# Performance work log

Hardware: AMD Instinct MI355X
Metric: run time of the kernel (lower is better)

Reference implementation:

```python
import jax, jax.numpy as jnp
import numpy as np

N_MODES = 64


def setup_inputs() -> dict:
    key = jax.random.key(0)
    k1, k2, k3 = jax.random.split(key, 3)
    B, Cin, S = 32, 128, 8192
    H, Hc, M = 4, 32, N_MODES  # n_heads, head_channels, n_modes (Cout = H*Hc = 128)
    x = jax.random.normal(k1, (B, Cin, S), dtype=jnp.float32)
    # per-head init scale: std = 0.01 * 2**h (matches _init_weights)
    scale = (0.01 * 2.0 ** jnp.arange(H, dtype=jnp.float32)).reshape(H, 1, 1, 1)
    w_real = jax.random.normal(k2, (H, Cin, Hc, M), dtype=jnp.float32) * scale
    w_imag = jax.random.normal(k3, (H, Cin, Hc, M), dtype=jnp.float32) * scale
    return {"x": x, "w_real": w_real, "w_imag": w_imag}


def reference(x, w_real, w_imag):
    B, Cin, S = x.shape
    H, _, Hc, M = w_real.shape
    Cout = H * Hc
    x_ft = jnp.fft.rfft(x, axis=-1)                 # [B, Cin, F] complex64
    F = x_ft.shape[-1]
    M = min(M, F)                                    # static
    w = (w_real + 1j * w_imag).astype(x_ft.dtype)    # [H, Cin, Hc, M]
    # fused batched complex contraction over all heads/modes at once
    out = jnp.einsum('bim,hiom->bhom', x_ft[:, :, :M], w[..., :M])  # [B, H, Hc, M]
    out = out.reshape(B, Cout, M)                    # head h -> channels [h*Hc, (h+1)*Hc)
    out_ft = jnp.zeros((B, Cout, F), dtype=x_ft.dtype).at[:, :, :M].set(out)
    return jnp.fft.irfft(out_ft, n=S, axis=-1)       # [B, Cout, S] float32
```

## Files before the change

### kernel.cpp

```cpp
#include <hip/hip_runtime.h>
#include <cstdio>

#define S_LEN 8192
#define NM 64

typedef short s8v __attribute__((ext_vector_type(8)));
typedef float f4  __attribute__((ext_vector_type(4)));
typedef _Float16 h8 __attribute__((ext_vector_type(8)));

static __device__ inline unsigned short f2bf(float f) {
    unsigned int u = __builtin_bit_cast(unsigned int, f);
    u = (u + 0x7FFFu + ((u >> 16) & 1u)) >> 16;
    return (unsigned short)u;
}
static __device__ inline float bf2f(unsigned short h) {
    unsigned int u = ((unsigned int)h) << 16;
    return __builtin_bit_cast(float, u);
}

#define SW32(r, k) (((r) * 32) + ((k) ^ ((((r) >> 1) & 3) << 3)))

static __device__ __forceinline__ void glds16(const void* g, void* l) {
    __builtin_amdgcn_global_load_lds(
        (const __attribute__((address_space(1))) unsigned int*)g,
        (__attribute__((address_space(3))) unsigned int*)l, 16, 0, 0);
}

__global__ __launch_bounds__(256) void gen_master(float* __restrict__ tab) {
    int p = blockIdx.x * 256 + threadIdx.x;
    tab[p] = cosf((float)p * (6.28318530717958647692f / (float)S_LEN));
}

__global__ __launch_bounds__(256) void gen_t1_img(const float* __restrict__ tab,
                                                  short* __restrict__ Th,
                                                  short* __restrict__ Tl) {
    int tid = blockIdx.x * 256 + threadIdx.x;
    int tile = tid >> 12;
    int sb = tile >> 2, kc = tile & 3;
    int us = tid & 4095;
    int ls = us >> 5, kx = us & 31;
    int lk = kx ^ (((ls >> 1) & 3) << 3);
    int s = sb * 128 + ls;
    int k = kc * 32 + lk;
    int m = k >> 1;
    int p = (m * s + ((k & 1) << 11)) & (S_LEN - 1);
    float v = tab[p];
    unsigned short h = f2bf(v);
    Th[tid] = (short)h;
    Tl[tid] = (short)f2bf(v - bf2f(h));
}

__global__ __launch_bounds__(256) void gen_b_img(const float* __restrict__ tab,
                                                 _Float16* __restrict__ Bimg) {
    int tid = blockIdx.x * 256 + threadIdx.x;
    int tk = tid >> 13;
    int us = tid & 8191;
    int c = us >> 6;
    int wl = us & 63;
    int slot = wl >> 3, e = wl & 7;
    int k = ((slot ^ (c & 7)) << 3) | e;
    int kg = tk * 64 + k;
    int m = c >> 1;
    int p = (m * kg + ((c & 1) << 11)) & (S_LEN - 1);
    Bimg[tid] = (_Float16)tab[p];
}

__global__ __launch_bounds__(512, 4) void dft_fwd_mfma(const float* __restrict__ x,
        const _Float16* __restrict__ Bimg, float* __restrict__ P) {
    __shared__ _Float16 abh[2][4096], abl[2][4096];
    __shared__ _Float16 bb[2][8192];
    const int t = threadIdx.x;
    const int lane = t & 63, w = t >> 6;
    const int rl = lane & 15, kq = lane >> 4;
    const int wr = w >> 2, wc = w & 3;
    const int row0 = blockIdx.x * 64;
    const int ks = blockIdx.y;
    const int rA = t >> 3, sA = t & 7;
    const size_t xrow = (size_t)(row0 + rA) * S_LEN + (size_t)ks * 1024 + (size_t)sA * 8;
    const int usA = rA * 64 + ((sA ^ (rA & 7)) << 3);
    const size_t bby = (size_t)ks * 16 * 16384 + (size_t)t * 32;

    f4 acc[2][2];
    #pragma unroll
    for (int i = 0; i < 2; ++i)
        #pragma unroll
        for (int j = 0; j < 2; ++j) acc[i][j] = (f4){0.f, 0.f, 0.f, 0.f};

    f4 aP[3][2];
    h8 bP[2][2];

    #define LA_(SC, A0, A1) { A0 = *(const f4*)&x[xrow + (size_t)(SC) * 64];       \
                              A1 = *(const f4*)&x[xrow + (size_t)(SC) * 64 + 4]; }
    #define LB_(SC, B0, B1) { const char* g = (const char*)Bimg + bby +            \
                                  (size_t)(SC) * 16384;                            \
                              B0 = *(const h8*)g; B1 = *(const h8*)(g + 16); }
    #define CV_(A0, A1, NXT) { h8 hv, lv;                                          \
        _Pragma("unroll")                                                          \
        for (int e = 0; e < 4; ++e) {                                              \
            float f = A0[e]; _Float16 hh = (_Float16)f;                            \
            hv[e] = hh; lv[e] = (_Float16)(f - (float)hh);                         \
        }                                                                          \
        _Pragma("unroll")                                                          \
        for (int e = 0; e < 4; ++e) {                                              \
            float f = A1[e]; _Float16 hh = (_Float16)f;                            \
            hv[4 + e] = hh; lv[4 + e] = (_Float16)(f - (float)hh);                 \
        }                                                                          \
        *(h8*)&abh[NXT][usA] = hv;                                                 \
        *(h8*)&abl[NXT][usA] = lv; }
    #define WB_(B0, B1, NXT) { *(h8*)&bb[NXT][t * 16] = B0;                        \
                               *(h8*)&bb[NXT][t * 16 + 8] = B1; }
    #define MM_(CUR) { _Pragma("unroll")                                           \
        for (int ksl = 0; ksl < 2; ++ksl) {                                        \
            const int sb_ = ksl * 4 + kq;                                          \
            h8 Ah0, Al0, Ah1, Al1, Bv0, Bv1;                                       \
            { int r = wr * 32 + rl;      int u = r * 64 + ((sb_ ^ (r & 7)) << 3);  \
              Ah0 = *(const h8*)&abh[CUR][u]; Al0 = *(const h8*)&abl[CUR][u]; }    \
            { int r = wr * 32 + 16 + rl; int u = r * 64 + ((sb_ ^ (r & 7)) << 3);  \
              Ah1 = *(const h8*)&abh[CUR][u]; Al1 = *(const h8*)&abl[CUR][u]; }    \
            { int c = wc * 32 + rl;      int u = c * 64 + ((sb_ ^ (c & 7)) << 3);  \
              Bv0 = *(const h8*)&bb[CUR][u]; }                                     \
            { int c = wc * 32 + 16 + rl; int u = c * 64 + ((sb_ ^ (c & 7)) << 3);  \
              Bv1 = *(const h8*)&bb[CUR][u]; }                                     \
            acc[0][0] = __builtin_amdgcn_mfma_f32_16x16x32_f16(Ah0, Bv0, acc[0][0], 0, 0, 0); \
            acc[0][1] = __builtin_amdgcn_mfma_f32_16x16x32_f16(Ah0, Bv1, acc[0][1], 0, 0, 0); \
            acc[1][0] = __builtin_amdgcn_mfma_f32_16x16x32_f16(Ah1, Bv0, acc[1][0], 0, 0, 0); \
            acc[1][1] = __builtin_amdgcn_mfma_f32_16x16x32_f16(Ah1, Bv1, acc[1][1], 0, 0, 0); \
            acc[0][0] = __builtin_amdgcn_mfma_f32_16x16x32_f16(Al0, Bv0, acc[0][0], 0, 0, 0); \
            acc[0][1] = __builtin_amdgcn_mfma_f32_16x16x32_f16(Al0, Bv1, acc[0][1], 0, 0, 0); \
            acc[1][0] = __builtin_amdgcn_mfma_f32_16x16x32_f16(Al1, Bv0, acc[1][0], 0, 0, 0); \
            acc[1][1] = __builtin_amdgcn_mfma_f32_16x16x32_f16(Al1, Bv1, acc[1][1], 0, 0, 0); \
        } }
    #define BAR_ __builtin_amdgcn_sched_barrier(0);                                \
        asm volatile("s_waitcnt lgkmcnt(0)" ::: "memory");                         \
        __builtin_amdgcn_sched_barrier(0);                                         \
        __builtin_amdgcn_s_barrier();                                              \
        __builtin_amdgcn_sched_barrier(0);

    {
        f4 t0a, t0b; h8 tb0a, tb0b;
        LA_(0, t0a, t0b) LB_(0, tb0a, tb0b)
        LA_(1, aP[1][0], aP[1][1]) LA_(2, aP[2][0], aP[2][1])
        LB_(1, bP[1][0], bP[1][1])
        __builtin_amdgcn_sched_barrier(0);
        CV_(t0a, t0b, 0) WB_(tb0a, tb0b, 0)
        BAR_
    }
    #pragma unroll
    for (int s = 0; s < 16; ++s) {
        if (s + 3 <= 15) LA_(s + 3, aP[(s + 3) % 3][0], aP[(s + 3) % 3][1])
        if (s + 2 <= 15) LB_(s + 2, bP[(s + 2) & 1][0], bP[(s + 2) & 1][1])
        __builtin_amdgcn_sched_barrier(0);
        if (s + 1 <= 15) { CV_(aP[(s + 1) % 3][0], aP[(s + 1) % 3][1], (s + 1) & 1)
                           WB_(bP[(s + 1) & 1][0], bP[(s + 1) & 1][1], (s + 1) & 1) }
        MM_(s & 1)
        if (s < 15) { BAR_ }
    }

    float* Pks = P + (size_t)ks * 524288;
    #pragma unroll
    for (int mf = 0; mf < 2; ++mf)
        #pragma unroll
        for (int nf = 0; nf < 2; ++nf)
            #pragma unroll
            for (int r = 0; r < 4; ++r)
                Pks[(size_t)(row0 + wr * 32 + mf * 16 + kq * 4 + r) * 128
                    + wc * 32 + nf * 16 + rl] = acc[mf][nf][r];
}

__global__ __launch_bounds__(256) void ksum(const float* __restrict__ P,
                                            float* __restrict__ X) {
    int i = (blockIdx.x * 256 + threadIdx.x) * 4;
    f4 s = (f4){0.f, 0.f, 0.f, 0.f};
    #pragma unroll
    for (int ks = 0; ks < 8; ++ks)
        s += *(const f4*)&P[(size_t)ks * 524288 + i];
    *(f4*)&X[i] = s;
}

__global__ __launch_bounds__(256) void mode_contract(const float* __restrict__ X,
        const float* __restrict__ w_real, const float* __restrict__ w_imag,
        short* __restrict__ C2h, short* __restrict__ C2l) {
    __shared__ float xr[32][128], xi[32][128];
    __shared__ float wr[128][32], wi[128][32];
    const int m = blockIdx.x, h = blockIdx.y, t = threadIdx.x;
    #pragma unroll
    for (int it = 0; it < 16; ++it) {
        int li = t + it * 256;
        int b = li >> 7, i = li & 127;
        const float2 v = *(const float2*)&X[(size_t)(b * 128 + i) * 128 + 2 * m];
        xr[b][i] = v.x; xi[b][i] = v.y;
        int i2 = li >> 5, o = li & 31;
        size_t off = ((size_t)((h * 128 + i2) * 32 + o)) * NM + m;
        wr[i2][o] = w_real[off];
        wi[i2][o] = w_imag[off];
    }
    __syncthreads();
    const int o = t & 31;
    const int b0 = (t >> 5) * 4;
    float re[4] = {0.f, 0.f, 0.f, 0.f}, im[4] = {0.f, 0.f, 0.f, 0.f};
    for (int i = 0; i < 128; ++i) {
        float wrv = wr[i][o], wiv = wi[i][o];
        #pragma unroll
        for (int j = 0; j < 4; ++j) {
            float a = xr[b0 + j][i], c = xi[b0 + j][i];
            re[j] += a * wrv - c * wiv;
            im[j] += a * wiv + c * wrv;
        }
    }
    const float alpha = (m == 0) ? (1.0f / (float)S_LEN) : (2.0f / (float)S_LEN);
    const int kc = m >> 4;
    const int lk = (2 * m) & 31;
    #pragma unroll
    for (int j = 0; j < 4; ++j) {
        int row = (b0 + j) * 128 + h * 32 + o;
        float vr = alpha * re[j], vi = alpha * im[j];
        unsigned short hr = f2bf(vr), hi_ = f2bf(vi);
        float lr = vr - bf2f(hr), li_ = vi - bf2f(hi_);
        int rb = row >> 7, lr_ = row & 127;
        size_t ui = ((size_t)(rb * 4 + kc) * 4096 + SW32(lr_, lk)) >> 1;
        ((unsigned int*)C2h)[ui] = ((unsigned int)hi_ << 16) | hr;
        ((unsigned int*)C2l)[ui] = ((unsigned int)f2bf(li_) << 16) | f2bf(lr);
    }
}

__global__ __launch_bounds__(256, 2) void idft_mfma(const short* __restrict__ C2h,
        const short* __restrict__ C2l, const short* __restrict__ T1h,
        const short* __restrict__ T1l, float* __restrict__ y) {
    __shared__ short ah[2][4096], al[2][4096];
    __shared__ short bh[2][4096], bl[2][4096];
    const int t = threadIdx.x;
    const int lane = t & 63, wid = t >> 6;
    const int wm = (wid >> 1) * 64, wn = (wid & 1) * 64;
    const int sb = blockIdx.x;
    const int rb = blockIdx.y;
    f4 acc[4][4];
    #pragma unroll
    for (int i = 0; i < 4; ++i)
        #pragma unroll
        for (int j = 0; j < 4; ++j) acc[i][j] = (f4){0.f, 0.f, 0.f, 0.f};

    #define DMA3(kc, buf)  {                                                       \
        const size_t ta = (size_t)(rb * 4 + (kc)) * 8192;                          \
        const size_t tb = (size_t)(sb * 4 + (kc)) * 8192;                          \
        const int wo = wid * 2048 + lane * 16;                                     \
        glds16((const char*)C2h + ta + wo,        (char*)&ah[buf][0] + wid * 2048);        \
        glds16((const char*)C2h + ta + wo + 1024, (char*)&ah[buf][0] + wid * 2048 + 1024); \
        glds16((const char*)C2l + ta + wo,        (char*)&al[buf][0] + wid * 2048);        \
        glds16((const char*)C2l + ta + wo + 1024, (char*)&al[buf][0] + wid * 2048 + 1024); \
        glds16((const char*)T1h + tb + wo,        (char*)&bh[buf][0] + wid * 2048);        \
        glds16((const char*)T1h + tb + wo + 1024, (char*)&bh[buf][0] + wid * 2048 + 1024); \
        glds16((const char*)T1l + tb + wo,        (char*)&bl[buf][0] + wid * 2048);        \
        glds16((const char*)T1l + tb + wo + 1024, (char*)&bl[buf][0] + wid * 2048 + 1024); }

    DMA3(0, 0);
    __syncthreads();
    #pragma unroll
    for (int kc = 0; kc < 4; ++kc) {
        const int cur = kc & 1;
        if (kc < 3) DMA3(kc + 1, cur ^ 1);
        {
            const int kk = (lane >> 4) * 8, rl = lane & 15;
            s8v Ah[4], Al[4], Bh[4], Bl[4];
            #pragma unroll
            for (int mf = 0; mf < 4; ++mf) {
                int us = SW32(wm + mf * 16 + rl, kk);
                Ah[mf] = *(const s8v*)&ah[cur][us];
                Al[mf] = *(const s8v*)&al[cur][us];
            }
            #pragma unroll
            for (int nf = 0; nf < 4; ++nf) {
                int us = SW32(wn + nf * 16 + rl, kk);
                Bh[nf] = *(const s8v*)&bh[cur][us];
                Bl[nf] = *(const s8v*)&bl[cur][us];
            }
            #pragma unroll
            for (int mf = 0; mf < 4; ++mf)
                #pragma unroll
                for (int nf = 0; nf < 4; ++nf)
                    acc[mf][nf] = __builtin_amdgcn_mfma_f32_16x16x32_bf16(Ah[mf], Bh[nf], acc[mf][nf], 0, 0, 0);
            #pragma unroll
            for (int mf = 0; mf < 4; ++mf)
                #pragma unroll
                for (int nf = 0; nf < 4; ++nf)
                    acc[mf][nf] = __builtin_amdgcn_mfma_f32_16x16x32_bf16(Al[mf], Bh[nf], acc[mf][nf], 0, 0, 0);
            #pragma unroll
            for (int mf = 0; mf < 4; ++mf)
                #pragma unroll
                for (int nf = 0; nf < 4; ++nf)
                    acc[mf][nf] = __builtin_amdgcn_mfma_f32_16x16x32_bf16(Ah[mf], Bl[nf], acc[mf][nf], 0, 0, 0);
        }
        __syncthreads();
    }
    #pragma unroll
    for (int mf = 0; mf < 4; ++mf) {
        int rr = rb * 128 + wm + mf * 16 + (lane >> 4) * 4;
        #pragma unroll
        for (int nf = 0; nf < 4; ++nf) {
            int c = sb * 128 + wn + nf * 16 + (lane & 15);
            #pragma unroll
            for (int r = 0; r < 4; ++r)
                __builtin_nontemporal_store(acc[mf][nf][r], &y[(size_t)(rr + r) * S_LEN + c]);
        }
    }
}

extern "C" void kernel_launch(void* const* d_in, const int* in_sizes, int n_in,
                              void* d_out, int out_size, void* d_ws, size_t ws_size,
                              hipStream_t stream) {
    const float* x      = (const float*)d_in[0];
    const float* w_real = (const float*)d_in[1];
    const float* w_imag = (const float*)d_in[2];
    float* y = (float*)d_out;

    const size_t TBL = (size_t)S_LEN * 128;
    char* w0 = (char*)d_ws;
    short* T1h     = (short*)w0;
    short* T1l     = T1h + TBL;
    _Float16* Bimg = (_Float16*)(T1l + TBL);
    float* X       = (float*)(Bimg + TBL);
    float* tab     = X + (size_t)4096 * 128;
    float* P       = tab + S_LEN;
    short* C2h     = (short*)P;
    short* C2l     = C2h + TBL;
    const size_t TOTAL = (size_t)((char*)(P + 8 * (size_t)4096 * 128) - w0);
    if (ws_size < TOTAL) {
        fprintf(stderr, "kernel_launch: ws too small (%zu < %zu bytes)\n", ws_size, TOTAL);
        return;
    }

    gen_master<<<S_LEN / 256, 256, 0, stream>>>(tab);
    gen_t1_img<<<(S_LEN * 128) / 256, 256, 0, stream>>>(tab, T1h, T1l);
    gen_b_img<<<(S_LEN * 128) / 256, 256, 0, stream>>>(tab, Bimg);
    dft_fwd_mfma<<<dim3(64, 8), 512, 0, stream>>>(x, Bimg, P);
    ksum<<<512, 256, 0, stream>>>(P, X);
    mode_contract<<<dim3(NM, 4), 256, 0, stream>>>(X, w_real, w_imag, C2h, C2l);
    idft_mfma<<<dim3(S_LEN / 128, 4096 / 128), 256, 0, stream>>>(C2h, C2l, T1h, T1l, y);
}
```

Before: 123.4 us.

## Drop LDS staging in forward DFT; load MFMA fragments directly from global

The twiddle table is regenerated in MFMA-fragment order, so each lane can load its B operand straight from global memory. The forward DFT kernel becomes a per-wave 16-row tile over all 128 columns, with no shared memory, barriers or manual software pipeline. Inputs are split into fp16 hi/lo halves in registers and fed to eight accumulators. This removes LDS traffic and barrier stalls, but every wave now rereads the full B tile through the caches, there are half as many threads per block, and latency hiding relies on the compiler unrolling the loop.

```diff
diff --git a/kernel.cpp b/kernel.cpp
--- a/kernel.cpp
+++ b/kernel.cpp
@@ -50,121 +50,69 @@
     Tl[tid] = (short)f2bf(v - bf2f(h));
 }
 
-__global__ __launch_bounds__(256) void gen_b_img(const float* __restrict__ tab,
-                                                 _Float16* __restrict__ Bimg) {
+__global__ __launch_bounds__(256) void gen_b_frag(const float* __restrict__ tab,
+                                                  _Float16* __restrict__ Bf) {
     int tid = blockIdx.x * 256 + threadIdx.x;
-    int tk = tid >> 13;
-    int us = tid & 8191;
-    int c = us >> 6;
-    int wl = us & 63;
-    int slot = wl >> 3, e = wl & 7;
-    int k = ((slot ^ (c & 7)) << 3) | e;
-    int kg = tk * 64 + k;
-    int m = c >> 1;
-    int p = (m * kg + ((c & 1) << 11)) & (S_LEN - 1);
-    Bimg[tid] = (_Float16)tab[p];
-}
-
-__global__ __launch_bounds__(512, 4) void dft_fwd_mfma(const float* __restrict__ x,
-        const _Float16* __restrict__ Bimg, float* __restrict__ P) {
-    __shared__ _Float16 abh[2][4096], abl[2][4096];
-    __shared__ _Float16 bb[2][8192];
+    int e = tid & 7;
+    int lane = (tid >> 3) & 63;
+    int nf = (tid >> 9) & 7;
+    int kstep = tid >> 12;
+    int rl = lane & 15, kq = lane >> 4;
+    int col = nf * 16 + rl;
+    int m = col >> 1;
+    int k = kstep * 32 + kq * 8 + e;
+    int p = (m * k + ((col & 1) << 11)) & (S_LEN - 1);
+    Bf[tid] = (_Float16)tab[p];
+}
+
+__global__ __launch_bounds__(256, 2) void dft_fwd_mfma(const float* __restrict__ x,
+        const _Float16* __restrict__ Bf, float* __restrict__ P) {
     const int t = threadIdx.x;
     const int lane = t & 63, w = t >> 6;
     const int rl = lane & 15, kq = lane >> 4;
-    const int wr = w >> 2, wc = w & 3;
-    const int row0 = blockIdx.x * 64;
+    const int mtile = blockIdx.x * 4 + w;
     const int ks = blockIdx.y;
-    const int rA = t >> 3, sA = t & 7;
-    const size_t xrow = (size_t)(row0 + rA) * S_LEN + (size_t)ks * 1024 + (size_t)sA * 8;
-    const int usA = rA * 64 + ((sA ^ (rA & 7)) << 3);
-    const size_t bby = (size_t)ks * 16 * 16384 + (size_t)t * 32;
-
-    f4 acc[2][2];
-    #pragma unroll
-    for (int i = 0; i < 2; ++i)
-        #pragma unroll
-        for (int j = 0; j < 2; ++j) acc[i][j] = (f4){0.f, 0.f, 0.f, 0.f};
-
-    f4 aP[3][2];
-    h8 bP[2][2];
-
-    #define LA_(SC, A0, A1) { A0 = *(const f4*)&x[xrow + (size_t)(SC) * 64];       \
-                              A1 = *(const f4*)&x[xrow + (size_t)(SC) * 64 + 4]; }
-    #define LB_(SC, B0, B1) { const char* g = (const char*)Bimg + bby +            \
-                                  (size_t)(SC) * 16384;                            \
-                              B0 = *(const h8*)g; B1 = *(const h8*)(g + 16); }
-    #define CV_(A0, A1, NXT) { h8 hv, lv;                                          \
-        _Pragma("unroll")                                                          \
-        for (int e = 0; e < 4; ++e) {                                              \
-            float f = A0[e]; _Float16 hh = (_Float16)f;                            \
-            hv[e] = hh; lv[e] = (_Float16)(f - (float)hh);                         \
-        }                                                                          \
-        _Pragma("unroll")                                                          \
-        for (int e = 0; e < 4; ++e) {                                              \
-            float f = A1[e]; _Float16 hh = (_Float16)f;                            \
-            hv[4 + e] = hh; lv[4 + e] = (_Float16)(f - (float)hh);                 \
-        }                                                                          \
-        *(h8*)&abh[NXT][usA] = hv;                                                 \
-        *(h8*)&abl[NXT][usA] = lv; }
-    #define WB_(B0, B1, NXT) { *(h8*)&bb[NXT][t * 16] = B0;                        \
-                               *(h8*)&bb[NXT][t * 16 + 8] = B1; }
-    #define MM_(CUR) { _Pragma("unroll")                                           \
-        for (int ksl = 0; ksl < 2; ++ksl) {                                        \
-            const int sb_ = ksl * 4 + kq;                                          \
-            h8 Ah0, Al0, Ah1, Al1, Bv0, Bv1;                                       \
-            { int r = wr * 32 + rl;      int u = r * 64 + ((sb_ ^ (r & 7)) << 3);  \
-              Ah0 = *(const h8*)&abh[CUR][u]; Al0 = *(const h8*)&abl[CUR][u]; }    \
-            { int r = wr * 32 + 16 + rl; int u = r * 64 + ((sb_ ^ (r & 7)) << 3);  \
-              Ah1 = *(const h8*)&abh[CUR][u]; Al1 = *(const h8*)&abl[CUR][u]; }    \
-            { int c = wc * 32 + rl;      int u = c * 64 + ((sb_ ^ (c & 7)) << 3);  \
-              Bv0 = *(const h8*)&bb[CUR][u]; }                                     \
-            { int c = wc * 32 + 16 + rl; int u = c * 64 + ((sb_ ^ (c & 7)) << 3);  \
-              Bv1 = *(const h8*)&bb[CUR][u]; }                                     \
-            acc[0][0] = __builtin_amdgcn_mfma_f32_16x16x32_f16(Ah0, Bv0, acc[0][0], 0, 0, 0); \
-            acc[0][1] = __builtin_amdgcn_mfma_f32_16x16x32_f16(Ah0, Bv1, acc[0][1], 0, 0, 0); \
-            acc[1][0] = __builtin_amdgcn_mfma_f32_16x16x32_f16(Ah1, Bv0, acc[1][0], 0, 0, 0); \
-            acc[1][1] = __builtin_amdgcn_mfma_f32_16x16x32_f16(Ah1, Bv1, acc[1][1], 0, 0, 0); \
-            acc[0][0] = __builtin_amdgcn_mfma_f32_16x16x32_f16(Al0, Bv0, acc[0][0], 0, 0, 0); \
-            acc[0][1] = __builtin_amdgcn_mfma_f32_16x16x32_f16(Al0, Bv1, acc[0][1], 0, 0, 0); \
-            acc[1][0] = __builtin_amdgcn_mfma_f32_16x16x32_f16(Al1, Bv0, acc[1][0], 0, 0, 0); \
-            acc[1][1] = __builtin_amdgcn_mfma_f32_16x16x32_f16(Al1, Bv1, acc[1][1], 0, 0, 0); \
-        } }
-    #define BAR_ __builtin_amdgcn_sched_barrier(0);                                \
-        asm volatile("s_waitcnt lgkmcnt(0)" ::: "memory");                         \
-        __builtin_amdgcn_sched_barrier(0);                                         \
-        __builtin_amdgcn_s_barrier();                                              \
-        __builtin_amdgcn_sched_barrier(0);
-
-    {
-        f4 t0a, t0b; h8 tb0a, tb0b;
-        LA_(0, t0a, t0b) LB_(0, tb0a, tb0b)
-        LA_(1, aP[1][0], aP[1][1]) LA_(2, aP[2][0], aP[2][1])
-        LB_(1, bP[1][0], bP[1][1])
-        __builtin_amdgcn_sched_barrier(0);
-        CV_(t0a, t0b, 0) WB_(tb0a, tb0b, 0)
-        BAR_
-    }
-    #pragma unroll
-    for (int s = 0; s < 16; ++s) {
-        if (s + 3 <= 15) LA_(s + 3, aP[(s + 3) % 3][0], aP[(s + 3) % 3][1])
-        if (s + 2 <= 15) LB_(s + 2, bP[(s + 2) & 1][0], bP[(s + 2) & 1][1])
-        __builtin_amdgcn_sched_barrier(0);
-        if (s + 1 <= 15) { CV_(aP[(s + 1) % 3][0], aP[(s + 1) % 3][1], (s + 1) & 1)
-                           WB_(bP[(s + 1) & 1][0], bP[(s + 1) & 1][1], (s + 1) & 1) }
-        MM_(s & 1)
-        if (s < 15) { BAR_ }
+    const int row0 = mtile * 16;
+    const size_t xbase = (size_t)(row0 + rl) * S_LEN + (size_t)ks * 1024 + (size_t)kq * 8;
+    const char* bbase = (const char*)Bf + (size_t)ks * 32 * 8192 + (size_t)lane * 16;
+
+    f4 acc[8];
+    #pragma unroll
+    for (int i = 0; i < 8; ++i) acc[i] = (f4){0.f, 0.f, 0.f, 0.f};
+
+    #pragma unroll
+    for (int s = 0; s < 32; ++s) {
+        f4 a0 = *(const f4*)&x[xbase + (size_t)s * 32];
+        f4 a1 = *(const f4*)&x[xbase + (size_t)s * 32 + 4];
+        h8 Bv[8];
+        #pragma unroll
+        for (int nf = 0; nf < 8; ++nf)
+            Bv[nf] = *(const h8*)(bbase + (size_t)s * 8192 + (size_t)nf * 1024);
+        h8 Ah, Al;
+        #pragma unroll
+        for (int e = 0; e < 4; ++e) {
+            float f = a0[e]; _Float16 hh = (_Float16)f;
+            Ah[e] = hh; Al[e] = (_Float16)(f - (float)hh);
+        }
+        #pragma unroll
+        for (int e = 0; e < 4; ++e) {
+            float f = a1[e]; _Float16 hh = (_Float16)f;
+            Ah[4 + e] = hh; Al[4 + e] = (_Float16)(f - (float)hh);
+        }
+        #pragma unroll
+        for (int nf = 0; nf < 8; ++nf)
+            acc[nf] = __builtin_amdgcn_mfma_f32_16x16x32_f16(Ah, Bv[nf], acc[nf], 0, 0, 0);
+        #pragma unroll
+        for (int nf = 0; nf < 8; ++nf)
+            acc[nf] = __builtin_amdgcn_mfma_f32_16x16x32_f16(Al, Bv[nf], acc[nf], 0, 0, 0);
     }
 
     float* Pks = P + (size_t)ks * 524288;
     #pragma unroll
-    for (int mf = 0; mf < 2; ++mf)
-        #pragma unroll
-        for (int nf = 0; nf < 2; ++nf)
-            #pragma unroll
-            for (int r = 0; r < 4; ++r)
-                Pks[(size_t)(row0 + wr * 32 + mf * 16 + kq * 4 + r) * 128
-                    + wc * 32 + nf * 16 + rl] = acc[mf][nf][r];
+    for (int nf = 0; nf < 8; ++nf)
+        #pragma unroll
+        for (int r = 0; r < 4; ++r)
+            Pks[(size_t)(row0 + kq * 4 + r) * 128 + nf * 16 + rl] = acc[nf][r];
 }
 
 __global__ __launch_bounds__(256) void ksum(const float* __restrict__ P,
@@ -316,8 +264,8 @@
     char* w0 = (char*)d_ws;
     short* T1h     = (short*)w0;
     short* T1l     = T1h + TBL;
-    _Float16* Bimg = (_Float16*)(T1l + TBL);
-    float* X       = (float*)(Bimg + TBL);
+    _Float16* Bf   = (_Float16*)(T1l + TBL);
+    float* X       = (float*)(Bf + TBL);
     float* tab     = X + (size_t)4096 * 128;
     float* P       = tab + S_LEN;
     short* C2h     = (short*)P;
@@ -330,8 +278,8 @@
 
     gen_master<<<S_LEN / 256, 256, 0, stream>>>(tab);
     gen_t1_img<<<(S_LEN * 128) / 256, 256, 0, stream>>>(tab, T1h, T1l);
-    gen_b_img<<<(S_LEN * 128) / 256, 256, 0, stream>>>(tab, Bimg);
-    dft_fwd_mfma<<<dim3(64, 8), 512, 0, stream>>>(x, Bimg, P);
+    gen_b_frag<<<(S_LEN * 128) / 256, 256, 0, stream>>>(tab, Bf);
+    dft_fwd_mfma<<<dim3(64, 8), 256, 0, stream>>>(x, Bf, P);
     ksum<<<512, 256, 0, stream>>>(P, X);
     mode_contract<<<dim3(NM, 4), 256, 0, stream>>>(X, w_real, w_imag, C2h, C2l);
     idft_mfma<<<dim3(S_LEN / 128, 4096 / 128), 256, 0, stream>>>(C2h, C2l, T1h, T1l, y);
```

Result: slower. 132.0 us (+7.0%).

## Drop hi/lo fp16 split of x in forward DFT and halve row tile

Applied to the files above, without the earlier changes.

The forward DFT kernel stops splitting x into high and low fp16 parts and uses a single fp16 conversion, which halves the MFMA count and the A-side shared memory. The row tile per block shrinks from 64 to 32 rows, the grid doubles, and the occupancy hint rises from 4 to 6 blocks. The aim is less matrix-core and LDS work plus more parallelism. The cost is precision: inputs rounded to fp16 without the residual term may push the forward DFT error past tolerance.

```diff
diff --git a/kernel.cpp b/kernel.cpp
--- a/kernel.cpp
+++ b/kernel.cpp
@@ -7,6 +7,7 @@
 typedef short s8v __attribute__((ext_vector_type(8)));
 typedef float f4  __attribute__((ext_vector_type(4)));
 typedef _Float16 h8 __attribute__((ext_vector_type(8)));
+typedef _Float16 h4 __attribute__((ext_vector_type(4)));
 
 static __device__ inline unsigned short f2bf(float f) {
     unsigned int u = __builtin_bit_cast(unsigned int, f);
@@ -65,71 +66,48 @@
     Bimg[tid] = (_Float16)tab[p];
 }
 
-__global__ __launch_bounds__(512, 4) void dft_fwd_mfma(const float* __restrict__ x,
+__global__ __launch_bounds__(512, 6) void dft_fwd_mfma(const float* __restrict__ x,
         const _Float16* __restrict__ Bimg, float* __restrict__ P) {
-    __shared__ _Float16 abh[2][4096], abl[2][4096];
+    __shared__ _Float16 ab[2][2048];
     __shared__ _Float16 bb[2][8192];
     const int t = threadIdx.x;
     const int lane = t & 63, w = t >> 6;
     const int rl = lane & 15, kq = lane >> 4;
     const int wr = w >> 2, wc = w & 3;
-    const int row0 = blockIdx.x * 64;
+    const int row0 = blockIdx.x * 32;
     const int ks = blockIdx.y;
-    const int rA = t >> 3, sA = t & 7;
-    const size_t xrow = (size_t)(row0 + rA) * S_LEN + (size_t)ks * 1024 + (size_t)sA * 8;
-    const int usA = rA * 64 + ((sA ^ (rA & 7)) << 3);
+    const int rA = t >> 4, kfA = (t & 15) * 4;
+    const size_t xrow = (size_t)(row0 + rA) * S_LEN + (size_t)ks * 1024 + kfA;
+    const int usA = rA * 64 + ((((kfA >> 3) ^ rA) & 7) << 3) + (kfA & 7);
     const size_t bby = (size_t)ks * 16 * 16384 + (size_t)t * 32;
 
-    f4 acc[2][2];
-    #pragma unroll
-    for (int i = 0; i < 2; ++i)
-        #pragma unroll
-        for (int j = 0; j < 2; ++j) acc[i][j] = (f4){0.f, 0.f, 0.f, 0.f};
-
-    f4 aP[3][2];
+    f4 acc[2];
+    acc[0] = (f4){0.f, 0.f, 0.f, 0.f};
+    acc[1] = (f4){0.f, 0.f, 0.f, 0.f};
+    f4 aP[3];
     h8 bP[2][2];
 
-    #define LA_(SC, A0, A1) { A0 = *(const f4*)&x[xrow + (size_t)(SC) * 64];       \
-                              A1 = *(const f4*)&x[xrow + (size_t)(SC) * 64 + 4]; }
+    #define LA_(SC, A0) { A0 = *(const f4*)&x[xrow + (size_t)(SC) * 64]; }
     #define LB_(SC, B0, B1) { const char* g = (const char*)Bimg + bby +            \
                                   (size_t)(SC) * 16384;                            \
                               B0 = *(const h8*)g; B1 = *(const h8*)(g + 16); }
-    #define CV_(A0, A1, NXT) { h8 hv, lv;                                          \
+    #define CV_(A0, NXT) { h4 hv;                                                  \
         _Pragma("unroll")                                                          \
-        for (int e = 0; e < 4; ++e) {                                              \
-            float f = A0[e]; _Float16 hh = (_Float16)f;                            \
-            hv[e] = hh; lv[e] = (_Float16)(f - (float)hh);                         \
-        }                                                                          \
-        _Pragma("unroll")                                                          \
-        for (int e = 0; e < 4; ++e) {                                              \
-            float f = A1[e]; _Float16 hh = (_Float16)f;                            \
-            hv[4 + e] = hh; lv[4 + e] = (_Float16)(f - (float)hh);                 \
-        }                                                                          \
-        *(h8*)&abh[NXT][usA] = hv;                                                 \
-        *(h8*)&abl[NXT][usA] = lv; }
+        for (int e = 0; e < 4; ++e) hv[e] = (_Float16)A0[e];                       \
+        *(h4*)&ab[NXT][usA] = hv; }
     #define WB_(B0, B1, NXT) { *(h8*)&bb[NXT][t * 16] = B0;                        \
                                *(h8*)&bb[NXT][t * 16 + 8] = B1; }
     #define MM_(CUR) { _Pragma("unroll")                                           \
         for (int ksl = 0; ksl < 2; ++ksl) {                                        \
-            const int sb_ = ksl * 4 + kq;                                          \
-            h8 Ah0, Al0, Ah1, Al1, Bv0, Bv1;                                       \
-            { int r = wr * 32 + rl;      int u = r * 64 + ((sb_ ^ (r & 7)) << 3);  \
-              Ah0 = *(const h8*)&abh[CUR][u]; Al0 = *(const h8*)&abl[CUR][u]; }    \
-            { int r = wr * 32 + 16 + rl; int u = r * 64 + ((sb_ ^ (r & 7)) << 3);  \
-              Ah1 = *(const h8*)&abh[CUR][u]; Al1 = *(const h8*)&abl[CUR][u]; }    \
-            { int c = wc * 32 + rl;      int u = c * 64 + ((sb_ ^ (c & 7)) << 3);  \
-              Bv0 = *(const h8*)&bb[CUR][u]; }                                     \
-            { int c = wc * 32 + 16 + rl; int u = c * 64 + ((sb_ ^ (c & 7)) << 3);  \
-              Bv1 = *(const h8*)&bb[CUR][u]; }                                     \
-            acc[0][0] = __builtin_amdgcn_mfma_f32_16x16x32_f16(Ah0, Bv0, acc[0][0], 0, 0, 0); \
-            acc[0][1] = __builtin_amdgcn_mfma_f32_16x16x32_f16(Ah0, Bv1, acc[0][1], 0, 0, 0); \
-            acc[1][0] = __builtin_amdgcn_mfma_f32_16x16x32_f16(Ah1, Bv0, acc[1][0], 0, 0, 0); \
-            acc[1][1] = __builtin_amdgcn_mfma_f32_16x16x32_f16(Ah1, Bv1, acc[1][1], 0, 0, 0); \
-            acc[0][0] = __builtin_amdgcn_mfma_f32_16x16x32_f16(Al0, Bv0, acc[0][0], 0, 0, 0); \
-            acc[0][1] = __builtin_amdgcn_mfma_f32_16x16x32_f16(Al0, Bv1, acc[0][1], 0, 0, 0); \
-            acc[1][0] = __builtin_amdgcn_mfma_f32_16x16x32_f16(Al1, Bv0, acc[1][0], 0, 0, 0); \
-            acc[1][1] = __builtin_amdgcn_mfma_f32_16x16x32_f16(Al1, Bv1, acc[1][1], 0, 0, 0); \
-        } }
+            const int slot = ksl * 4 + kq;                                         \
+            const int r = wr * 16 + rl;                                            \
+            h8 Av = *(const h8*)&ab[CUR][r * 64 + ((slot ^ (r & 7)) << 3)];        \
+            _Pragma("unroll")                                                      \
+            for (int nf = 0; nf < 2; ++nf) {                                       \
+                const int c = wc * 32 + nf * 16 + rl;                              \
+                h8 Bv = *(const h8*)&bb[CUR][c * 64 + ((slot ^ (c & 7)) << 3)];    \
+                acc[nf] = __builtin_amdgcn_mfma_f32_16x16x32_f16(Av, Bv, acc[nf], 0, 0, 0); \
+            } } }
     #define BAR_ __builtin_amdgcn_sched_barrier(0);                                \
         asm volatile("s_waitcnt lgkmcnt(0)" ::: "memory");                         \
         __builtin_amdgcn_sched_barrier(0);                                         \
@@ -137,20 +115,20 @@
         __builtin_amdgcn_sched_barrier(0);
 
     {
-        f4 t0a, t0b; h8 tb0a, tb0b;
-        LA_(0, t0a, t0b) LB_(0, tb0a, tb0b)
-        LA_(1, aP[1][0], aP[1][1]) LA_(2, aP[2][0], aP[2][1])
+        f4 t0a; h8 tb0a, tb0b;
+        LA_(0, t0a) LB_(0, tb0a, tb0b)
+        LA_(1, aP[1]) LA_(2, aP[2])
         LB_(1, bP[1][0], bP[1][1])
         __builtin_amdgcn_sched_barrier(0);
-        CV_(t0a, t0b, 0) WB_(tb0a, tb0b, 0)
+        CV_(t0a, 0) WB_(tb0a, tb0b, 0)
         BAR_
     }
     #pragma unroll
     for (int s = 0; s < 16; ++s) {
-        if (s + 3 <= 15) LA_(s + 3, aP[(s + 3) % 3][0], aP[(s + 3) % 3][1])
+        if (s + 3 <= 15) LA_(s + 3, aP[(s + 3) % 3])
         if (s + 2 <= 15) LB_(s + 2, bP[(s + 2) & 1][0], bP[(s + 2) & 1][1])
         __builtin_amdgcn_sched_barrier(0);
-        if (s + 1 <= 15) { CV_(aP[(s + 1) % 3][0], aP[(s + 1) % 3][1], (s + 1) & 1)
+        if (s + 1 <= 15) { CV_(aP[(s + 1) % 3], (s + 1) & 1)
                            WB_(bP[(s + 1) & 1][0], bP[(s + 1) & 1][1], (s + 1) & 1) }
         MM_(s & 1)
         if (s < 15) { BAR_ }
@@ -158,13 +136,11 @@
 
     float* Pks = P + (size_t)ks * 524288;
     #pragma unroll
-    for (int mf = 0; mf < 2; ++mf)
+    for (int nf = 0; nf < 2; ++nf)
         #pragma unroll
-        for (int nf = 0; nf < 2; ++nf)
-            #pragma unroll
-            for (int r = 0; r < 4; ++r)
-                Pks[(size_t)(row0 + wr * 32 + mf * 16 + kq * 4 + r) * 128
-                    + wc * 32 + nf * 16 + rl] = acc[mf][nf][r];
+        for (int r = 0; r < 4; ++r)
+            Pks[(size_t)(row0 + wr * 16 + kq * 4 + r) * 128
+                + wc * 32 + nf * 16 + rl] = acc[nf][r];
 }
 
 __global__ __launch_bounds__(256) void ksum(const float* __restrict__ P,
@@ -331,7 +307,7 @@
     gen_master<<<S_LEN / 256, 256, 0, stream>>>(tab);
     gen_t1_img<<<(S_LEN * 128) / 256, 256, 0, stream>>>(tab, T1h, T1l);
     gen_b_img<<<(S_LEN * 128) / 256, 256, 0, stream>>>(tab, Bimg);
-    dft_fwd_mfma<<<dim3(64, 8), 512, 0, stream>>>(x, Bimg, P);
+    dft_fwd_mfma<<<dim3(128, 8), 512, 0, stream>>>(x, Bimg, P);
     ksum<<<512, 256, 0, stream>>>(P, X);
     mode_contract<<<dim3(NM, 4), 256, 0, stream>>>(X, w_real, w_imag, C2h, C2l);
     idft_mfma<<<dim3(S_LEN / 128, 4096 / 128), 256, 0, stream>>>(C2h, C2l, T1h, T1l, y);
```

After: 124.1 us. Within noise of the previous version (+0.5%).
